# Optimization experiments

Measured on AMD Instinct MI355X. Metric: run time of the kernel, lower is better.

## Reference

```python
import jax, jax.numpy as jnp
import numpy as np

B, T, C = 2, 2048, 1024
H = 16
HD = C // H  # head_size = 64


def setup_inputs() -> dict:
    key = jax.random.key(0)
    k1, k2, k3 = jax.random.split(key, 3)
    x = jax.random.normal(k1, (B, T, C), dtype=jnp.float32)
    W_qkv = jax.random.normal(k2, (C, 3 * C), dtype=jnp.float32) * (1.0 / np.sqrt(C))
    b_qkv = jnp.zeros((3 * C,), dtype=jnp.float32)
    W_proj = jax.random.normal(k3, (C, C), dtype=jnp.float32) * (1.0 / np.sqrt(C))
    b_proj = jnp.zeros((C,), dtype=jnp.float32)
    return {"x": x, "W_qkv": W_qkv, "b_qkv": b_qkv, "W_proj": W_proj, "b_proj": b_proj}


def reference(x, W_qkv, b_qkv, W_proj, b_proj):
    Bc, Tc, Cc = x.shape
    qkv = x @ W_qkv + b_qkv                      # [B,T,3C]
    # Faithful to torch: view(B,T,H,3*HD) then chunk(3,-1) -> per-head interleaved split
    qkv = qkv.reshape(Bc, Tc, H, 3 * HD)
    q = qkv[..., 0 * HD:1 * HD]                  # [B,T,H,HD]
    k = qkv[..., 1 * HD:2 * HD]
    v = qkv[..., 2 * HD:3 * HD]
    # scores: [B,H,T,T]
    att = jnp.einsum('bqhd,bkhd->bhqk', q, k) / np.sqrt(HD)
    causal = jnp.tril(jnp.ones((Tc, Tc), dtype=bool))
    att = jnp.where(causal[None, None, :, :], att, -jnp.inf)
    att = jax.nn.softmax(att, axis=-1)
    out = jnp.einsum('bhqk,bkhd->bqhd', att, v).reshape(Bc, Tc, Cc)
    return out @ W_proj + b_proj
```

## Files before the change

kernel.cpp:

```cpp
#include <hip/hip_runtime.h>
#include <hip/hip_bf16.h>
#include <stdint.h>
#include <math.h>

#define T_SEQ 2048
#define NHEAD 16
#define CDIM 1024
#define QKV2_LD 2048

typedef __attribute__((ext_vector_type(8))) short short8;
typedef __attribute__((ext_vector_type(4))) short short4v;
typedef __attribute__((ext_vector_type(4))) float floatx4;

static __device__ __forceinline__ short bf16b(float f) {
    __hip_bfloat16 h = __float2bfloat16(f);
    return __builtin_bit_cast(short, h);
}

__global__ __launch_bounds__(256) void convert_f32_bf16(
    const float* __restrict__ in, __hip_bfloat16* __restrict__ out, int n)
{
    int i = (blockIdx.x * 256 + threadIdx.x) * 8;
    if (i >= n) return;
    float4 a = *(const float4*)(in + i);
    float4 b = *(const float4*)(in + i + 4);
    short8 o;
    o[0] = bf16b(a.x); o[1] = bf16b(a.y); o[2] = bf16b(a.z); o[3] = bf16b(a.w);
    o[4] = bf16b(b.x); o[5] = bf16b(b.y); o[6] = bf16b(b.z); o[7] = bf16b(b.w);
    *(short8*)(out + i) = o;
}

__global__ __launch_bounds__(256) void transpose_convert_kernel(
    const float* __restrict__ in, __hip_bfloat16* __restrict__ out,
    int R, int C)
{
    __shared__ short tile[64][65];
    const int r0 = blockIdx.y << 6;
    const int c0 = blockIdx.x << 6;
    const int tid = threadIdx.x;
    #pragma unroll
    for (int t = 0; t < 4; ++t) {
        int ch = t * 256 + tid;
        int rr = ch >> 4, cc = (ch & 15) << 2;
        float4 v = *(const float4*)(in + (size_t)(r0 + rr) * C + c0 + cc);
        tile[rr][cc + 0] = bf16b(v.x);
        tile[rr][cc + 1] = bf16b(v.y);
        tile[rr][cc + 2] = bf16b(v.z);
        tile[rr][cc + 3] = bf16b(v.w);
    }
    __syncthreads();
    #pragma unroll
    for (int t = 0; t < 2; ++t) {
        int ch = t * 256 + tid;
        int cc = ch >> 3, rr8 = (ch & 7) << 3;
        short8 v;
        #pragma unroll
        for (int j = 0; j < 8; ++j) v[j] = tile[rr8 + j][cc];
        *(short8*)(out + (size_t)(c0 + cc) * R + r0 + rr8) = v;
    }
}

template <int MI, int NI, int MINW, bool QKV, typename OutT>
__global__ __launch_bounds__(256, MINW) void gemm_bias_kernel(
    const __hip_bfloat16* __restrict__ A,
    const __hip_bfloat16* __restrict__ Bt,
    const float* __restrict__ bias,
    OutT* __restrict__ C,
    __hip_bfloat16* __restrict__ vT,
    int M, int N, int K)
{
    __shared__ short As[MI * 32 * 64];
    __shared__ short Bs[NI * 32 * 64];
    const int tid  = threadIdx.x;
    const int lane = tid & 63;
    const int w    = tid >> 6;
    const int quad = lane >> 4;
    const int c16  = lane & 15;
    const int m0 = blockIdx.x * (MI * 32);
    const int n0 = blockIdx.y * (NI * 32);
    const int wm = (w >> 1) * (MI * 16);
    const int wn = (w & 1) * (NI * 16);

    floatx4 acc[MI][NI] = {};

    for (int kt = 0; kt < K; kt += 64) {
        __syncthreads();
        #pragma unroll
        for (int r = 0; r < MI; ++r) {
            int ch = r * 256 + tid;
            int row = ch >> 3, k8 = (ch & 7) << 3;
            const __hip_bfloat16* ga = A + (size_t)(m0 + row) * K + kt + k8;
            __builtin_amdgcn_global_load_lds(
                (const __attribute__((address_space(1))) void*)ga,
                (__attribute__((address_space(3))) void*)&As[ch * 8], 16, 0, 0);
        }
        #pragma unroll
        for (int r = 0; r < NI; ++r) {
            int ch = r * 256 + tid;
            int row = ch >> 3, k8 = (ch & 7) << 3;
            const __hip_bfloat16* gb = Bt + (size_t)(n0 + row) * K + kt + k8;
            __builtin_amdgcn_global_load_lds(
                (const __attribute__((address_space(1))) void*)gb,
                (__attribute__((address_space(3))) void*)&Bs[ch * 8], 16, 0, 0);
        }
        __syncthreads();
        #pragma unroll
        for (int ko = 0; ko < 64; ko += 32) {
            short8 af[MI], bfr[NI];
            #pragma unroll
            for (int mi = 0; mi < MI; ++mi)
                af[mi] = *(const short8*)&As[(wm + mi * 16 + c16) * 64 + ko + quad * 8];
            #pragma unroll
            for (int ni = 0; ni < NI; ++ni)
                bfr[ni] = *(const short8*)&Bs[(wn + ni * 16 + c16) * 64 + ko + quad * 8];
            #pragma unroll
            for (int mi = 0; mi < MI; ++mi)
                #pragma unroll
                for (int ni = 0; ni < NI; ++ni)
                    acc[mi][ni] = __builtin_amdgcn_mfma_f32_16x16x32_bf16(
                        af[mi], bfr[ni], acc[mi][ni], 0, 0, 0);
        }
    }

    if constexpr (QKV) {
        const int colblk = (n0 + wn) >> 6;
        const int head = colblk / 3;
        const int kind = colblk % 3;
        const int b    = m0 >> 11;
        if (kind == 2) {
            const size_t vbase = ((size_t)(b * 16 + head)) * 64 * T_SEQ;
            #pragma unroll
            for (int mi = 0; mi < MI; ++mi) {
                int t0 = ((m0 + wm + mi * 16) & 2047) + quad * 4;
                #pragma unroll
                for (int ni = 0; ni < NI; ++ni) {
                    int hd = ni * 16 + c16;
                    float bv = bias[n0 + wn + hd];
                    short4v pk;
                    #pragma unroll
                    for (int r2 = 0; r2 < 4; ++r2)
                        pk[r2] = bf16b(acc[mi][ni][r2] + bv);
                    *(short4v*)(vT + vbase + (size_t)hd * T_SEQ + t0) = pk;
                }
            }
        } else {
            const int cbase = head * 128 + kind * 64;
            #pragma unroll
            for (int mi = 0; mi < MI; ++mi)
                #pragma unroll
                for (int ni = 0; ni < NI; ++ni) {
                    float bv = bias[n0 + wn + ni * 16 + c16];
                    int col = cbase + ni * 16 + c16;
                    #pragma unroll
                    for (int r2 = 0; r2 < 4; ++r2) {
                        int row = m0 + wm + mi * 16 + quad * 4 + r2;
                        C[(size_t)row * QKV2_LD + col] = __float2bfloat16(acc[mi][ni][r2] + bv);
                    }
                }
        }
    } else {
        #pragma unroll
        for (int mi = 0; mi < MI; ++mi)
            #pragma unroll
            for (int ni = 0; ni < NI; ++ni) {
                int col = n0 + wn + ni * 16 + c16;
                float bv = bias[col];
                #pragma unroll
                for (int r2 = 0; r2 < 4; ++r2) {
                    int row = m0 + wm + mi * 16 + quad * 4 + r2;
                    float v = acc[mi][ni][r2] + bv;
                    if constexpr (__is_same(OutT, float)) {
                        C[(size_t)row * N + col] = v;
                    } else {
                        C[(size_t)row * N + col] = __float2bfloat16(v);
                    }
                }
            }
    }
}

__global__ __launch_bounds__(256, 2) void attn_kernel(
    const __hip_bfloat16* __restrict__ qkv,
    const __hip_bfloat16* __restrict__ vT,
    __hip_bfloat16* __restrict__ attn_out)
{
    __shared__ short Ks[2][64 * 64];
    __shared__ short Vs[2][64 * 64];
    __shared__ short Pl[4][2][16 * 64];

    const int hb = blockIdx.x;
    const int p  = blockIdx.y;
    const int h  = hb & 15;
    const int b  = hb >> 4;
    const int tid  = threadIdx.x;
    const int lane = tid & 63;
    const int w    = tid >> 6;
    const int quad = lane >> 4;
    const int c16  = lane & 15;

    const size_t rowbase = (size_t)b * T_SEQ;
    const size_t vbase   = (size_t)hb * 64 * T_SEQ;
    const int qtA = p, qtB = 31 - p;
    const int q0A = qtA << 6, q0B = qtB << 6;
    const int wrow = w << 4;
    const int hoff = h * 128;
    const int key  = c16 & 7;

    short8 qfA[2], qfB[2];
    #pragma unroll
    for (int ko = 0; ko < 2; ++ko) {
        qfA[ko] = *(const short8*)(qkv +
            (rowbase + q0A + wrow + c16) * QKV2_LD + hoff + ko * 32 + quad * 8);
        qfB[ko] = *(const short8*)(qkv +
            (rowbase + q0B + wrow + c16) * QKV2_LD + hoff + ko * 32 + quad * 8);
    }

    floatx4 OA[4] = {}, OB[4] = {};
    float lpA = 0.f, lpB = 0.f;
    const float sc = 0.125f * 1.4426950408889634f;
    const int nkt = qtB + 1;

    auto stage = [&](int kt, int bsel) {
        const int k0s = kt << 6;
        #pragma unroll
        for (int r = 0; r < 2; ++r) {
            int ch = r * 256 + tid;
            int krow = ch >> 3;
            int hc = (ch & 7) ^ (krow & 7);
            const __hip_bfloat16* g = qkv + (rowbase + k0s + krow) * QKV2_LD + hoff + 64 + hc * 8;
            __builtin_amdgcn_global_load_lds(
                (const __attribute__((address_space(1))) void*)g,
                (__attribute__((address_space(3))) void*)&Ks[bsel][ch * 8], 16, 0, 0);
        }
        #pragma unroll
        for (int r = 0; r < 2; ++r) {
            int ch = r * 256 + tid;
            int hd = ch >> 3;
            int kc = (ch & 7) ^ (hd & 7);
            const __hip_bfloat16* g = vT + vbase + (size_t)hd * T_SEQ + k0s + kc * 8;
            __builtin_amdgcn_global_load_lds(
                (const __attribute__((address_space(1))) void*)g,
                (__attribute__((address_space(3))) void*)&Vs[bsel][ch * 8], 16, 0, 0);
        }
    };

    stage(0, 0);
    int buf = 0;

    for (int kt = 0; kt < nkt; ++kt) {
        __syncthreads();
        if (kt + 1 < nkt) stage(kt + 1, buf ^ 1);

        short8 kf[2][4], vb[2][4];
        #pragma unroll
        for (int ko = 0; ko < 2; ++ko)
            #pragma unroll
            for (int ni = 0; ni < 4; ++ni) {
                int sl = ((4 * ko + quad) ^ key) << 3;
                kf[ko][ni] = *(const short8*)&Ks[buf][(ni * 16 + c16) * 64 + sl];
                vb[ko][ni] = *(const short8*)&Vs[buf][(ni * 16 + c16) * 64 + sl];
            }

        auto process = [&](const short8 (&qf)[2], floatx4 (&O)[4], float& lp,
                           bool diag, short* Pw) {
            floatx4 S[4] = {};
            #pragma unroll
            for (int ko = 0; ko < 2; ++ko)
                #pragma unroll
                for (int ni = 0; ni < 4; ++ni)
                    S[ni] = __builtin_amdgcn_mfma_f32_16x16x32_bf16(
                        kf[ko][ni], qf[ko], S[ni], 0, 0, 0);
            if (diag) {
                #pragma unroll
                for (int ni = 0; ni < 4; ++ni)
                    #pragma unroll
                    for (int r = 0; r < 4; ++r) {
                        bool msk = (ni * 16 + quad * 4 + r) > (wrow + c16);
                        float pe = msk ? 0.f : exp2f(S[ni][r] * sc);
                        S[ni][r] = pe;
                        lp += pe;
                    }
            } else {
                #pragma unroll
                for (int ni = 0; ni < 4; ++ni)
                    #pragma unroll
                    for (int r = 0; r < 4; ++r) {
                        float pe = exp2f(S[ni][r] * sc);
                        S[ni][r] = pe;
                        lp += pe;
                    }
            }
            #pragma unroll
            for (int ni = 0; ni < 4; ++ni) {
                short4v pk;
                #pragma unroll
                for (int r = 0; r < 4; ++r) pk[r] = bf16b(S[ni][r]);
                int pair = ni * 2 + (quad >> 1);
                int off = c16 * 64 + ((((pair ^ key) << 1) + (quad & 1)) << 2);
                *(short4v*)&Pw[off] = pk;
            }
            #pragma unroll
            for (int ko = 0; ko < 2; ++ko) {
                int off = c16 * 64 + (((ko * 4 + quad) ^ key) << 3);
                short8 pa = *(const short8*)&Pw[off];
                #pragma unroll
                for (int ni = 0; ni < 4; ++ni)
                    O[ni] = __builtin_amdgcn_mfma_f32_16x16x32_bf16(
                        vb[ko][ni], pa, O[ni], 0, 0, 0);
            }
        };

        process(qfB, OB, lpB, kt == qtB, &Pl[w][1][0]);
        if (kt <= qtA) process(qfA, OA, lpA, kt == qtA, &Pl[w][0][0]);
        buf ^= 1;
    }

    auto finish = [&](floatx4 (&O)[4], float lp, int q0) {
        float l = lp;
        l += __shfl_xor(l, 16);
        l += __shfl_xor(l, 32);
        float inv = 1.0f / l;
        size_t row = rowbase + q0 + wrow + c16;
        #pragma unroll
        for (int ni = 0; ni < 4; ++ni) {
            short4v o;
            #pragma unroll
            for (int r = 0; r < 4; ++r) o[r] = bf16b(O[ni][r] * inv);
            *(short4v*)(attn_out + row * CDIM + h * 64 + ni * 16 + quad * 4) = o;
        }
    };
    finish(OA, lpA, q0A);
    finish(OB, lpB, q0B);
}

extern "C" void kernel_launch(void* const* d_in, const int* in_sizes, int n_in,
                              void* d_out, int out_size, void* d_ws, size_t ws_size,
                              hipStream_t stream) {
    const float* x     = (const float*)d_in[0];
    const float* Wqkv  = (const float*)d_in[1];
    const float* bqkv  = (const float*)d_in[2];
    const float* Wproj = (const float*)d_in[3];
    const float* bproj = (const float*)d_in[4];
    float* out = (float*)d_out;

    __hip_bfloat16* xb     = (__hip_bfloat16*)d_ws;
    __hip_bfloat16* WqkvT  = xb     + (size_t)4096 * 1024;
    __hip_bfloat16* WprojT = WqkvT  + (size_t)3072 * 1024;
    __hip_bfloat16* qkv2   = WprojT + (size_t)1024 * 1024;
    __hip_bfloat16* vT     = qkv2   + (size_t)4096 * 2048;
    __hip_bfloat16* attn   = vT     + (size_t)32 * 64 * 2048;

    convert_f32_bf16<<<4096 * 1024 / 2048, 256, 0, stream>>>(x, xb, 4096 * 1024);
    transpose_convert_kernel<<<dim3(3072 / 64, 1024 / 64), 256, 0, stream>>>(Wqkv, WqkvT, 1024, 3072);
    transpose_convert_kernel<<<dim3(1024 / 64, 1024 / 64), 256, 0, stream>>>(Wproj, WprojT, 1024, 1024);
    gemm_bias_kernel<4, 4, 2, true, __hip_bfloat16>
        <<<dim3(4096 / 128, 3072 / 128), 256, 0, stream>>>(
        xb, WqkvT, bqkv, qkv2, vT, 4096, 3072, 1024);
    attn_kernel<<<dim3(32, 16), 256, 0, stream>>>(qkv2, vT, attn);
    gemm_bias_kernel<4, 2, 2, false, float>
        <<<dim3(4096 / 128, 1024 / 64), 256, 0, stream>>>(
        attn, WprojT, bproj, out, nullptr, 4096, 1024, 1024);
}
```

Before: 181.9 us.

## Fuse prep kernels, stage V transpose through LDS, shrink P scratch, retile proj GEMM

Three fp32-to-bf16 conversion and transpose launches are merged into one prep kernel. The V-transposed epilogue of the QKV GEMM now goes through a swizzled LDS tile, so global writes become coalesced 16-byte rows instead of scattered 8-byte stores. The attention kernel shares one P scratch buffer per wave between its two query tiles, which cuts LDS use. The output projection GEMM switches to 64x64 tiles with a higher occupancy target, giving more blocks. The extra __syncthreads and the LDS round trip add some cost to the GEMM epilogue.

```diff
diff --git a/kernel.cpp b/kernel.cpp
--- a/kernel.cpp
+++ b/kernel.cpp
@@ -17,27 +17,13 @@
     return __builtin_bit_cast(short, h);
 }
 
-__global__ __launch_bounds__(256) void convert_f32_bf16(
-    const float* __restrict__ in, __hip_bfloat16* __restrict__ out, int n)
-{
-    int i = (blockIdx.x * 256 + threadIdx.x) * 8;
-    if (i >= n) return;
-    float4 a = *(const float4*)(in + i);
-    float4 b = *(const float4*)(in + i + 4);
-    short8 o;
-    o[0] = bf16b(a.x); o[1] = bf16b(a.y); o[2] = bf16b(a.z); o[3] = bf16b(a.w);
-    o[4] = bf16b(b.x); o[5] = bf16b(b.y); o[6] = bf16b(b.z); o[7] = bf16b(b.w);
-    *(short8*)(out + i) = o;
-}
-
-__global__ __launch_bounds__(256) void transpose_convert_kernel(
+__device__ __forceinline__ void transpose_body(
     const float* __restrict__ in, __hip_bfloat16* __restrict__ out,
-    int R, int C)
+    int R, int C, int bx, int by, int tid)
 {
     __shared__ short tile[64][65];
-    const int r0 = blockIdx.y << 6;
-    const int c0 = blockIdx.x << 6;
-    const int tid = threadIdx.x;
+    const int r0 = by << 6;
+    const int c0 = bx << 6;
     #pragma unroll
     for (int t = 0; t < 4; ++t) {
         int ch = t * 256 + tid;
@@ -57,6 +43,30 @@
         #pragma unroll
         for (int j = 0; j < 8; ++j) v[j] = tile[rr8 + j][cc];
         *(short8*)(out + (size_t)(c0 + cc) * R + r0 + rr8) = v;
+    }
+}
+
+__global__ __launch_bounds__(256) void prep_kernel(
+    const float* __restrict__ x,     __hip_bfloat16* __restrict__ xb,
+    const float* __restrict__ Wqkv,  __hip_bfloat16* __restrict__ WqkvT,
+    const float* __restrict__ Wproj, __hip_bfloat16* __restrict__ WprojT)
+{
+    const int bid = blockIdx.x;
+    const int tid = threadIdx.x;
+    if (bid < 2048) {
+        int i = (bid * 256 + tid) * 8;
+        float4 a = *(const float4*)(x + i);
+        float4 b = *(const float4*)(x + i + 4);
+        short8 o;
+        o[0] = bf16b(a.x); o[1] = bf16b(a.y); o[2] = bf16b(a.z); o[3] = bf16b(a.w);
+        o[4] = bf16b(b.x); o[5] = bf16b(b.y); o[6] = bf16b(b.z); o[7] = bf16b(b.w);
+        *(short8*)(xb + i) = o;
+    } else if (bid < 2816) {
+        int r = bid - 2048;
+        transpose_body(Wqkv, WqkvT, 1024, 3072, r % 48, r / 48, tid);
+    } else {
+        int r = bid - 2816;
+        transpose_body(Wproj, WprojT, 1024, 1024, r & 15, r >> 4, tid);
     }
 }
 
@@ -127,21 +137,29 @@
         const int head = colblk / 3;
         const int kind = colblk % 3;
         const int b    = m0 >> 11;
+        __syncthreads();
         if (kind == 2) {
-            const size_t vbase = ((size_t)(b * 16 + head)) * 64 * T_SEQ;
-            #pragma unroll
-            for (int mi = 0; mi < MI; ++mi) {
-                int t0 = ((m0 + wm + mi * 16) & 2047) + quad * 4;
+            short* tp = (w < 2) ? &As[w * 4096] : &Bs[(w - 2) * 4096];
+            #pragma unroll
+            for (int mi = 0; mi < MI; ++mi)
                 #pragma unroll
                 for (int ni = 0; ni < NI; ++ni) {
                     int hd = ni * 16 + c16;
                     float bv = bias[n0 + wn + hd];
                     short4v pk;
                     #pragma unroll
-                    for (int r2 = 0; r2 < 4; ++r2)
-                        pk[r2] = bf16b(acc[mi][ni][r2] + bv);
-                    *(short4v*)(vT + vbase + (size_t)hd * T_SEQ + t0) = pk;
+                    for (int r2 = 0; r2 < 4; ++r2) pk[r2] = bf16b(acc[mi][ni][r2] + bv);
+                    int tc = mi * 4 + quad;
+                    *(short4v*)&tp[hd * 64 + ((tc ^ ((hd & 7) << 1)) << 2)] = pk;
                 }
+            const size_t vb2 = ((size_t)(b * 16 + head)) * 64 * T_SEQ;
+            const int t0 = (m0 + wm) & 2047;
+            #pragma unroll
+            for (int it = 0; it < 8; ++it) {
+                int hd = it * 8 + (lane >> 3);
+                int tc2 = (lane & 7) << 1;
+                short8 vv = *(const short8*)&tp[hd * 64 + ((tc2 ^ ((hd & 7) << 1)) << 2)];
+                *(short8*)(vT + vb2 + (size_t)hd * T_SEQ + t0 + ((lane & 7) << 3)) = vv;
             }
         } else {
             const int cbase = head * 128 + kind * 64;
@@ -186,7 +204,7 @@
 {
     __shared__ short Ks[2][64 * 64];
     __shared__ short Vs[2][64 * 64];
-    __shared__ short Pl[4][2][16 * 64];
+    __shared__ short Pl[4][16 * 64];
 
     const int hb = blockIdx.x;
     const int p  = blockIdx.y;
@@ -261,8 +279,8 @@
                 vb[ko][ni] = *(const short8*)&Vs[buf][(ni * 16 + c16) * 64 + sl];
             }
 
-        auto process = [&](const short8 (&qf)[2], floatx4 (&O)[4], float& lp,
-                           bool diag, short* Pw) {
+        auto process = [&](const short8 (&qf)[2], floatx4 (&O)[4], float& lp, bool diag) {
+            short* Pw = &Pl[w][0];
             floatx4 S[4] = {};
             #pragma unroll
             for (int ko = 0; ko < 2; ++ko)
@@ -310,8 +328,8 @@
             }
         };
 
-        process(qfB, OB, lpB, kt == qtB, &Pl[w][1][0]);
-        if (kt <= qtA) process(qfA, OA, lpA, kt == qtA, &Pl[w][0][0]);
+        process(qfB, OB, lpB, kt == qtB);
+        if (kt <= qtA) process(qfA, OA, lpA, kt == qtA);
         buf ^= 1;
     }
 
@@ -350,14 +368,12 @@
     __hip_bfloat16* vT     = qkv2   + (size_t)4096 * 2048;
     __hip_bfloat16* attn   = vT     + (size_t)32 * 64 * 2048;
 
-    convert_f32_bf16<<<4096 * 1024 / 2048, 256, 0, stream>>>(x, xb, 4096 * 1024);
-    transpose_convert_kernel<<<dim3(3072 / 64, 1024 / 64), 256, 0, stream>>>(Wqkv, WqkvT, 1024, 3072);
-    transpose_convert_kernel<<<dim3(1024 / 64, 1024 / 64), 256, 0, stream>>>(Wproj, WprojT, 1024, 1024);
+    prep_kernel<<<3072, 256, 0, stream>>>(x, xb, Wqkv, WqkvT, Wproj, WprojT);
     gemm_bias_kernel<4, 4, 2, true, __hip_bfloat16>
         <<<dim3(4096 / 128, 3072 / 128), 256, 0, stream>>>(
         xb, WqkvT, bqkv, qkv2, vT, 4096, 3072, 1024);
     attn_kernel<<<dim3(32, 16), 256, 0, stream>>>(qkv2, vT, attn);
-    gemm_bias_kernel<4, 2, 2, false, float>
-        <<<dim3(4096 / 128, 1024 / 64), 256, 0, stream>>>(
+    gemm_bias_kernel<2, 2, 4, false, float>
+        <<<dim3(4096 / 64, 1024 / 64), 256, 0, stream>>>(
         attn, WprojT, bproj, out, nullptr, 4096, 1024, 1024);
 }
```

Measured after the change: 178.0 us. 2.1% less time.
